# Kernel tuning notes

Hardware: AMD Instinct MI355X
Metric: run time of the kernel (lower is better)

Reference implementation:

```python
import jax, jax.numpy as jnp
import numpy as np

N_NODES = 100000
N_EDGES = 1600000
NUM_FEATURES = 256
HIDDEN_DIM = 128
NUM_CLASSES = 16


def setup_inputs() -> dict:
    key = jax.random.key(0)
    k1, k2, k3, k4 = jax.random.split(key, 4)
    x = jax.random.normal(k1, (N_NODES, NUM_FEATURES), dtype=jnp.float32)
    edge_index = jax.random.randint(k2, (2, N_EDGES), 0, N_NODES, dtype=jnp.int64)
    # Glorot-style init like PyG GCNConv's Linear
    W1 = jax.random.normal(k3, (NUM_FEATURES, HIDDEN_DIM), dtype=jnp.float32) / np.sqrt(NUM_FEATURES)
    b1 = jnp.zeros((HIDDEN_DIM,), dtype=jnp.float32)
    W2 = jax.random.normal(k4, (HIDDEN_DIM, NUM_CLASSES), dtype=jnp.float32) / np.sqrt(HIDDEN_DIM)
    b2 = jnp.zeros((NUM_CLASSES,), dtype=jnp.float32)
    return {"x": x, "edge_index": edge_index, "W1": W1, "b1": b1, "W2": W2, "b2": b2}


def _gcn_norm(edge_index, num_nodes):
    """PyG GCNConv default: add self-loops, symmetric deg^{-1/2} A deg^{-1/2} norm."""
    loops = jnp.arange(num_nodes, dtype=edge_index.dtype)
    row = jnp.concatenate([edge_index[0], loops])  # source
    col = jnp.concatenate([edge_index[1], loops])  # target
    deg = jax.ops.segment_sum(jnp.ones_like(col, dtype=jnp.float32), col,
                              num_segments=num_nodes)
    dinv = jnp.where(deg > 0, jax.lax.rsqrt(deg), 0.0)
    norm = dinv[row] * dinv[col]  # [E + N]
    return row, col, norm


def _gcn_conv(h, row, col, norm, num_nodes):
    # transform first (PyG: lin then propagate), then normalized sum-aggregate
    msg = h[row] * norm[:, None]            # [E+N, d] gather + scale
    return jax.ops.segment_sum(msg, col, num_segments=num_nodes)


def reference(x, edge_index, W1, b1, W2, b2):
    num_nodes = x.shape[0]
    row, col, norm = _gcn_norm(edge_index, num_nodes)
    h = x @ W1
    h = _gcn_conv(h, row, col, norm, num_nodes) + b1
    h = jax.nn.relu(h)
    h = h @ W2
    out = _gcn_conv(h, row, col, norm, num_nodes) + b2
    return out
```

## Files before the change

kernel.cpp:

```cpp
#include <hip/hip_runtime.h>

#define N_NODES 100000
#define N_EDGES 1600000
#define F_IN    256
#define F_HID   128
#define F_OUT   16

#define BSHIFT  9
#define BNODES  512
#define NB      196
#define ECAP    16384
#define CHUNK   4096
#define NCHUNK  ((N_EDGES + CHUNK - 1) / CHUNK)

typedef __attribute__((ext_vector_type(8))) short short8;
typedef __attribute__((ext_vector_type(4))) float float4v;

__device__ __forceinline__ unsigned int bf16_rn(float f) {
    unsigned int u = __float_as_uint(f);
    return (u + 0x7FFFu + ((u >> 16) & 1u)) >> 16;
}
__device__ __forceinline__ unsigned int cvtpk(float lo, float hi) {
    unsigned int r;
    asm("v_cvt_pk_bf16_f32 %0, %1, %2" : "=v"(r) : "v"(lo), "v"(hi));
    return r;
}
__device__ __forceinline__ float blo(unsigned int u) { return __uint_as_float(u << 16); }
__device__ __forceinline__ float bhi(unsigned int u) { return __uint_as_float(u & 0xFFFF0000u); }
__device__ __forceinline__ float bfu(unsigned short u) { return __uint_as_float(((unsigned int)u) << 16); }


__global__ __launch_bounds__(256) void k_binit(int* __restrict__ bcur) {
    int i = threadIdx.x;
    if (i < NB) bcur[i] = i * ECAP;
}

__global__ __launch_bounds__(256) void k_binscatter(const int* __restrict__ rowi,
                                                    const int* __restrict__ coli,
                                                    int* __restrict__ bcur,
                                                    unsigned int* __restrict__ ebuf) {
    __shared__ int cnt[NB], gbase[NB], run[NB];
    int tid = threadIdx.x;
    int e0 = blockIdx.x * CHUNK;
    for (int i = tid; i < NB; i += 256) { cnt[i] = 0; run[i] = 0; }
    __syncthreads();
    int d[16], s[16];
    #pragma unroll
    for (int i = 0; i < 16; i++) {
        int e = e0 + i * 256 + tid;
        if (e < N_EDGES) {
            d[i] = coli[e]; s[i] = rowi[e];
            atomicAdd(&cnt[d[i] >> BSHIFT], 1);
        } else d[i] = -1;
    }
    __syncthreads();
    for (int i = tid; i < NB; i += 256)
        gbase[i] = cnt[i] ? atomicAdd(&bcur[i], cnt[i]) : 0;
    __syncthreads();
    #pragma unroll
    for (int i = 0; i < 16; i++) {
        if (d[i] >= 0) {
            int b = d[i] >> BSHIFT;
            int off = atomicAdd(&run[b], 1);
            ebuf[gbase[b] + off] = ((unsigned int)(d[i] & 511) << 17) | (unsigned int)s[i];
        }
    }
}

__global__ __launch_bounds__(512) void k_finalize(const int* __restrict__ bcur,
                                                  const unsigned int* __restrict__ ebuf,
                                                  int* __restrict__ rp_start,
                                                  int* __restrict__ rp_end,
                                                  float* __restrict__ dinv,
                                                  int* __restrict__ esrc) {
    __shared__ int ndeg[BNODES];
    __shared__ int sc[BNODES];
    int tid = threadIdx.x;
    int b   = blockIdx.x;
    int nb0 = b << BSHIFT;
    int ebeg = b * ECAP, eend = bcur[b];
    ndeg[tid] = 0;
    __syncthreads();
    for (int e = ebeg + tid; e < eend; e += 512)
        atomicAdd(&ndeg[ebuf[e] >> 17], 1);
    __syncthreads();
    sc[tid] = ndeg[tid];
    __syncthreads();
    for (int off = 1; off < BNODES; off <<= 1) {
        int v = (tid >= off) ? sc[tid - off] : 0;
        __syncthreads();
        sc[tid] += v;
        __syncthreads();
    }
    {
        int n = nb0 + tid;
        int deg = ndeg[tid];
        int excl = sc[tid] - deg;
        if (n < N_NODES) {
            rp_start[n] = ebeg + excl;
            rp_end[n]   = ebeg + excl + deg;
            dinv[n]     = rsqrtf(1.0f + (float)deg);
        }
        ndeg[tid] = excl;
    }
    __syncthreads();
    for (int e = ebeg + tid; e < eend; e += 512) {
        unsigned int p = ebuf[e];
        int off = atomicAdd(&ndeg[p >> 17], 1);
        esrc[ebeg + off] = (int)(p & 0x1FFFFu);
    }
}


__global__ __launch_bounds__(256) void k_transW(const float* __restrict__ W1,
                                                ushort* __restrict__ Wt) {
    int t = blockIdx.x * 256 + threadIdx.x;
    int c = t & 127, k = t >> 7;
    Wt[c * 256 + k] = (ushort)cvtpk(W1[k * 128 + c], 0.f);
}


__global__ __launch_bounds__(256) void k_gemm1(const float* __restrict__ x,
                                               const ushort* __restrict__ Wt,
                                               const float* __restrict__ dinv,
                                               ushort* __restrict__ g1) {
    __shared__ ushort Bl[128 * 256];
    const int tid = threadIdx.x;
    const int w = tid >> 6;
    const int l = tid & 63;
    const int m = l & 15;
    const int q = l >> 4;
    const int R0 = blockIdx.x * 128;

    {
        const uint4* Wg = (const uint4*)Wt;
        uint4* Bl4 = (uint4*)Bl;
        #pragma unroll
        for (int it = 0; it < 16; it++) {
            int i = it * 256 + tid;
            int c = i >> 5, j = i & 31;
            Bl4[c * 32 + (j ^ (c & 7))] = Wg[i];
        }
    }
    __syncthreads();

    int r0 = R0 + w * 32 + m;      if (r0 > N_NODES - 1) r0 = N_NODES - 1;
    int r1 = R0 + w * 32 + 16 + m; if (r1 > N_NODES - 1) r1 = N_NODES - 1;
    const float* xr0 = &x[(size_t)r0 * F_IN + q * 8];
    const float* xr1 = &x[(size_t)r1 * F_IN + q * 8];
    const short8* Bl8 = (const short8*)Bl;

    float4v acc[2][8];
    #pragma unroll
    for (int i = 0; i < 2; i++)
        #pragma unroll
        for (int j = 0; j < 8; j++) acc[i][j] = (float4v){0.f, 0.f, 0.f, 0.f};

    #pragma unroll 2
    for (int kt = 0; kt < F_IN; kt += 32) {
        float4 a0 = *(const float4*)&xr0[kt];
        float4 a1 = *(const float4*)&xr0[kt + 4];
        float4 b0 = *(const float4*)&xr1[kt];
        float4 b1 = *(const float4*)&xr1[kt + 4];
        short8 af0, af1;
        ((uint*)&af0)[0] = cvtpk(a0.x, a0.y); ((uint*)&af0)[1] = cvtpk(a0.z, a0.w);
        ((uint*)&af0)[2] = cvtpk(a1.x, a1.y); ((uint*)&af0)[3] = cvtpk(a1.z, a1.w);
        ((uint*)&af1)[0] = cvtpk(b0.x, b0.y); ((uint*)&af1)[1] = cvtpk(b0.z, b0.w);
        ((uint*)&af1)[2] = cvtpk(b1.x, b1.y); ((uint*)&af1)[3] = cvtpk(b1.z, b1.w);
        int jq = (kt >> 3) + q;
        #pragma unroll
        for (int n = 0; n < 8; n++) {
            int col = n * 16 + m;
            short8 bfr = Bl8[col * 32 + (jq ^ (col & 7))];
            acc[0][n] = __builtin_amdgcn_mfma_f32_16x16x32_bf16(af0, bfr, acc[0][n], 0, 0, 0);
            acc[1][n] = __builtin_amdgcn_mfma_f32_16x16x32_bf16(af1, bfr, acc[1][n], 0, 0, 0);
        }
    }

    const int rbase = R0 + w * 32 + q * 4;
    float dv0[4], dv1[4];
    #pragma unroll
    for (int r = 0; r < 4; r++) {
        int v0 = rbase + r;      dv0[r] = (v0 < N_NODES) ? dinv[v0] : 0.f;
        int v1 = rbase + 16 + r; dv1[r] = (v1 < N_NODES) ? dinv[v1] : 0.f;
    }
    #pragma unroll
    for (int n = 0; n < 8; n++) {
        #pragma unroll
        for (int r = 0; r < 4; r++) {
            int v0 = rbase + r;
            if (v0 < N_NODES) {
                float f = dv0[r] * acc[0][n][r];
                g1[v0 * F_HID + n * 16 + m] = (ushort)cvtpk(f, f);
            }
            int v1 = rbase + 16 + r;
            if (v1 < N_NODES) {
                float f = dv1[r] * acc[1][n][r];
                g1[v1 * F_HID + n * 16 + m] = (ushort)cvtpk(f, f);
            }
        }
    }
}


__global__ __launch_bounds__(256) void k_agg1g2(const int* __restrict__ rp_start,
                                                const int* __restrict__ rp_end,
                                                const int* __restrict__ esrc,
                                                const float* __restrict__ dinv,
                                                const unsigned int* __restrict__ g1,
                                                const float* __restrict__ b1,
                                                const float* __restrict__ W2,
                                                ushort* __restrict__ g2b,
                                                int nbase) {
    __shared__ float hl[4][132];
    const int tid  = threadIdx.x;
    const int wave = tid >> 6;
    const int lane = tid & 63;
    const int col  = lane & 15, part = lane >> 4;

    float w2r[32];
    #pragma unroll
    for (int i = 0; i < 32; i++) w2r[i] = W2[i * 64 + lane];

    float2 bb = ((const float2*)b1)[lane];

    #pragma unroll 1
    for (int j = 0; j < 4; j++) {
        const int node = nbase + blockIdx.x * 16 + j * 4 + wave;
        int s = rp_start[node], t = rp_end[node];
        unsigned int u = g1[node * 64 + lane];
        float ax = blo(u), ay = bhi(u);
        int e = s;
        for (; e + 7 < t; e += 8) {
            int r0 = esrc[e],     r1 = esrc[e + 1], r2 = esrc[e + 2], r3 = esrc[e + 3];
            int r4 = esrc[e + 4], r5 = esrc[e + 5], r6 = esrc[e + 6], r7 = esrc[e + 7];
            unsigned int u0 = g1[r0 * 64 + lane], u1 = g1[r1 * 64 + lane];
            unsigned int u2 = g1[r2 * 64 + lane], u3 = g1[r3 * 64 + lane];
            unsigned int u4 = g1[r4 * 64 + lane], u5 = g1[r5 * 64 + lane];
            unsigned int u6 = g1[r6 * 64 + lane], u7 = g1[r7 * 64 + lane];
            ax += blo(u0) + blo(u1) + blo(u2) + blo(u3)
                + blo(u4) + blo(u5) + blo(u6) + blo(u7);
            ay += bhi(u0) + bhi(u1) + bhi(u2) + bhi(u3)
                + bhi(u4) + bhi(u5) + bhi(u6) + bhi(u7);
        }
        for (; e + 3 < t; e += 4) {
            int r0 = esrc[e], r1 = esrc[e + 1], r2 = esrc[e + 2], r3 = esrc[e + 3];
            unsigned int u0 = g1[r0 * 64 + lane], u1 = g1[r1 * 64 + lane];
            unsigned int u2 = g1[r2 * 64 + lane], u3 = g1[r3 * 64 + lane];
            ax += blo(u0) + blo(u1) + blo(u2) + blo(u3);
            ay += bhi(u0) + bhi(u1) + bhi(u2) + bhi(u3);
        }
        for (; e < t; e++) {
            unsigned int u0 = g1[esrc[e] * 64 + lane];
            ax += blo(u0); ay += bhi(u0);
        }
        float wv = dinv[node];
        hl[wave][lane * 2]     = fmaxf(fmaf(wv, ax, bb.x), 0.0f);
        hl[wave][lane * 2 + 1] = fmaxf(fmaf(wv, ay, bb.y), 0.0f);

        float acc = 0.f;
        #pragma unroll
        for (int i = 0; i < 32; i++)
            acc = fmaf(hl[wave][i * 4 + part], w2r[i], acc);
        acc += __shfl_xor(acc, 16);
        acc += __shfl_xor(acc, 32);
        if (lane < 16) g2b[node * 16 + col] = (ushort)bf16_rn(wv * acc);
    }
}


__global__ __launch_bounds__(256) void k_agg2(const int* __restrict__ rp_start,
                                              const int* __restrict__ rp_end,
                                              const int* __restrict__ esrc,
                                              const float* __restrict__ dinv,
                                              const ushort* __restrict__ g2b,
                                              const float* __restrict__ b2,
                                              float* __restrict__ out) {
    int gid = blockIdx.x * 256 + threadIdx.x;
    int node = gid >> 4;
    int f = gid & 15;
    if (node >= N_NODES) return;
    int s = rp_start[node], t = rp_end[node];
    float acc = bfu(g2b[node * 16 + f]);
    int e = s;
    for (; e + 7 < t; e += 8) {
        float a0 = bfu(g2b[esrc[e] * 16 + f]),     a1 = bfu(g2b[esrc[e + 1] * 16 + f]);
        float a2 = bfu(g2b[esrc[e + 2] * 16 + f]), a3 = bfu(g2b[esrc[e + 3] * 16 + f]);
        float a4 = bfu(g2b[esrc[e + 4] * 16 + f]), a5 = bfu(g2b[esrc[e + 5] * 16 + f]);
        float a6 = bfu(g2b[esrc[e + 6] * 16 + f]), a7 = bfu(g2b[esrc[e + 7] * 16 + f]);
        acc += a0 + a1 + a2 + a3 + a4 + a5 + a6 + a7;
    }
    for (; e + 3 < t; e += 4) {
        acc += bfu(g2b[esrc[e] * 16 + f]) + bfu(g2b[esrc[e + 1] * 16 + f])
             + bfu(g2b[esrc[e + 2] * 16 + f]) + bfu(g2b[esrc[e + 3] * 16 + f]);
    }
    for (; e < t; e++) acc += bfu(g2b[esrc[e] * 16 + f]);
    out[node * 16 + f] = fmaf(dinv[node], acc, b2[f]);
}


extern "C" void kernel_launch(void* const* d_in, const int* in_sizes, int n_in,
                              void* d_out, int out_size, void* d_ws, size_t ws_size,
                              hipStream_t stream) {
    const float* x   = (const float*)d_in[0];
    const int*   ei  = (const int*)d_in[1];
    const float* W1  = (const float*)d_in[2];
    const float* b1  = (const float*)d_in[3];
    const float* W2  = (const float*)d_in[4];
    const float* b2  = (const float*)d_in[5];
    float* out = (float*)d_out;

    const int* rowi = ei;
    const int* coli = ei + N_EDGES;

    char* ws = (char*)d_ws;
    int*          bcur     = (int*)(ws + 0);
    int*          rp_start = (int*)(ws + 8192);
    int*          rp_end   = (int*)(ws + 524288);
    float*        dinv     = (float*)(ws + 1048576);
    unsigned int* ebuf     = (unsigned int*)(ws + 2097152);
    int*          esrc     = (int*)(ws + 16777216);
    ushort*       Wt       = (ushort*)(ws + 31457280);
    ushort*       g1       = (ushort*)(ws + 33554432);
    ushort*       g2b      = (ushort*)(ws + 62914560);

    k_binit     <<<1, 256, 0, stream>>>(bcur);
    k_binscatter<<<NCHUNK, 256, 0, stream>>>(rowi, coli, bcur, ebuf);
    k_finalize  <<<NB, 512, 0, stream>>>(bcur, ebuf, rp_start, rp_end, dinv, esrc);
    k_transW    <<<128, 256, 0, stream>>>(W1, Wt);

    k_gemm1     <<<(N_NODES + 127) / 128, 256, 0, stream>>>(x, Wt, dinv, g1);
    k_agg1g2    <<<N_NODES / 32, 256, 0, stream>>>(rp_start, rp_end, esrc, dinv,
                                                   (const unsigned int*)g1, b1, W2, g2b, 0);
    k_agg1g2    <<<N_NODES / 32, 256, 0, stream>>>(rp_start, rp_end, esrc, dinv,
                                                   (const unsigned int*)g1, b1, W2, g2b,
                                                   N_NODES / 2);
    k_agg2      <<<(N_NODES * 16 + 255) / 256, 256, 0, stream>>>(rp_start, rp_end, esrc,
                                                                 dinv, g2b, b2, out);
}
```

Measured before the change: 327.9 us.

## Stage x tiles into LDS with async double-buffered loads, keep W1 in registers

The first GEMM now streams x tiles into a double-buffered, XOR-swizzled LDS buffer using global_load_lds, prefetching the next K slice while MFMAs run on the current one. Each wave holds its 32-column slice of W1 in registers instead of staging all of W1 in LDS, and the work is repartitioned so each wave covers all 128 rows for 32 output columns. The aim is to hide the x-load latency and shrink LDS use so more blocks fit per CU. The cost is a barrier per K step and higher register pressure from the 16 W fragments plus 16 accumulators.

```diff
diff --git a/kernel.cpp b/kernel.cpp
--- a/kernel.cpp
+++ b/kernel.cpp
@@ -15,6 +15,9 @@
 
 typedef __attribute__((ext_vector_type(8))) short short8;
 typedef __attribute__((ext_vector_type(4))) float float4v;
+
+typedef __attribute__((address_space(1))) const void g_void;
+typedef __attribute__((address_space(3))) void lds_void;
 
 __device__ __forceinline__ unsigned int bf16_rn(float f) {
     unsigned int u = __float_as_uint(f);
@@ -124,79 +127,80 @@
                                                const ushort* __restrict__ Wt,
                                                const float* __restrict__ dinv,
                                                ushort* __restrict__ g1) {
-    __shared__ ushort Bl[128 * 256];
+    __shared__ float lx[2][128][32];
     const int tid = threadIdx.x;
-    const int w = tid >> 6;
-    const int l = tid & 63;
-    const int m = l & 15;
-    const int q = l >> 4;
+    const int wv = tid >> 6;
+    const int l  = tid & 63;
+    const int m  = l & 15;
+    const int q  = l >> 4;
     const int R0 = blockIdx.x * 128;
 
-    {
-        const uint4* Wg = (const uint4*)Wt;
-        uint4* Bl4 = (uint4*)Bl;
+    #pragma unroll
+    for (int r = 0; r < 4; r++) {
+        int rt = r * 32 + wv * 8 + (l >> 3);
+        int c16 = l & 7;
+        int grow = R0 + rt; if (grow > N_NODES - 1) grow = N_NODES - 1;
+        const float* src = x + (size_t)grow * F_IN + ((c16 ^ (rt & 7)) << 2);
+        float* dst = &lx[0][r * 32 + wv * 8][0];
+        __builtin_amdgcn_global_load_lds((g_void*)src, (lds_void*)dst, 16, 0, 0);
+    }
+
+    short8 wf[2][8];
+    #pragma unroll
+    for (int ng = 0; ng < 2; ng++)
         #pragma unroll
-        for (int it = 0; it < 16; it++) {
-            int i = it * 256 + tid;
-            int c = i >> 5, j = i & 31;
-            Bl4[c * 32 + (j ^ (c & 7))] = Wg[i];
-        }
-    }
-    __syncthreads();
-
-    int r0 = R0 + w * 32 + m;      if (r0 > N_NODES - 1) r0 = N_NODES - 1;
-    int r1 = R0 + w * 32 + 16 + m; if (r1 > N_NODES - 1) r1 = N_NODES - 1;
-    const float* xr0 = &x[(size_t)r0 * F_IN + q * 8];
-    const float* xr1 = &x[(size_t)r1 * F_IN + q * 8];
-    const short8* Bl8 = (const short8*)Bl;
-
-    float4v acc[2][8];
-    #pragma unroll
-    for (int i = 0; i < 2; i++)
+        for (int kt = 0; kt < 8; kt++)
+            wf[ng][kt] = *(const short8*)&Wt[(wv * 32 + ng * 16 + m) * 256 + kt * 32 + q * 8];
+
+    float4v acc[8][2];
+    #pragma unroll
+    for (int rg = 0; rg < 8; rg++) {
+        acc[rg][0] = (float4v){0.f, 0.f, 0.f, 0.f};
+        acc[rg][1] = (float4v){0.f, 0.f, 0.f, 0.f};
+    }
+
+    __syncthreads();
+
+    #pragma unroll
+    for (int kt = 0; kt < 8; kt++) {
+        const int buf = kt & 1;
+        if (kt < 7) {
+            #pragma unroll
+            for (int r = 0; r < 4; r++) {
+                int rt = r * 32 + wv * 8 + (l >> 3);
+                int c16 = l & 7;
+                int grow = R0 + rt; if (grow > N_NODES - 1) grow = N_NODES - 1;
+                const float* src = x + (size_t)grow * F_IN + (kt + 1) * 32
+                                     + ((c16 ^ (rt & 7)) << 2);
+                float* dst = &lx[buf ^ 1][r * 32 + wv * 8][0];
+                __builtin_amdgcn_global_load_lds((g_void*)src, (lds_void*)dst, 16, 0, 0);
+            }
+        }
         #pragma unroll
-        for (int j = 0; j < 8; j++) acc[i][j] = (float4v){0.f, 0.f, 0.f, 0.f};
-
-    #pragma unroll 2
-    for (int kt = 0; kt < F_IN; kt += 32) {
-        float4 a0 = *(const float4*)&xr0[kt];
-        float4 a1 = *(const float4*)&xr0[kt + 4];
-        float4 b0 = *(const float4*)&xr1[kt];
-        float4 b1 = *(const float4*)&xr1[kt + 4];
-        short8 af0, af1;
-        ((uint*)&af0)[0] = cvtpk(a0.x, a0.y); ((uint*)&af0)[1] = cvtpk(a0.z, a0.w);
-        ((uint*)&af0)[2] = cvtpk(a1.x, a1.y); ((uint*)&af0)[3] = cvtpk(a1.z, a1.w);
-        ((uint*)&af1)[0] = cvtpk(b0.x, b0.y); ((uint*)&af1)[1] = cvtpk(b0.z, b0.w);
-        ((uint*)&af1)[2] = cvtpk(b1.x, b1.y); ((uint*)&af1)[3] = cvtpk(b1.z, b1.w);
-        int jq = (kt >> 3) + q;
-        #pragma unroll
-        for (int n = 0; n < 8; n++) {
-            int col = n * 16 + m;
-            short8 bfr = Bl8[col * 32 + (jq ^ (col & 7))];
-            acc[0][n] = __builtin_amdgcn_mfma_f32_16x16x32_bf16(af0, bfr, acc[0][n], 0, 0, 0);
-            acc[1][n] = __builtin_amdgcn_mfma_f32_16x16x32_bf16(af1, bfr, acc[1][n], 0, 0, 0);
-        }
-    }
-
-    const int rbase = R0 + w * 32 + q * 4;
-    float dv0[4], dv1[4];
-    #pragma unroll
-    for (int r = 0; r < 4; r++) {
-        int v0 = rbase + r;      dv0[r] = (v0 < N_NODES) ? dinv[v0] : 0.f;
-        int v1 = rbase + 16 + r; dv1[r] = (v1 < N_NODES) ? dinv[v1] : 0.f;
-    }
-    #pragma unroll
-    for (int n = 0; n < 8; n++) {
+        for (int rg = 0; rg < 8; rg++) {
+            int rt = rg * 16 + m, sw = rt & 7;
+            float4 e0 = *(const float4*)&lx[buf][rt][((2 * q)     ^ sw) * 4];
+            float4 e1 = *(const float4*)&lx[buf][rt][((2 * q + 1) ^ sw) * 4];
+            short8 af;
+            ((uint*)&af)[0] = cvtpk(e0.x, e0.y); ((uint*)&af)[1] = cvtpk(e0.z, e0.w);
+            ((uint*)&af)[2] = cvtpk(e1.x, e1.y); ((uint*)&af)[3] = cvtpk(e1.z, e1.w);
+            acc[rg][0] = __builtin_amdgcn_mfma_f32_16x16x32_bf16(af, wf[0][kt], acc[rg][0], 0, 0, 0);
+            acc[rg][1] = __builtin_amdgcn_mfma_f32_16x16x32_bf16(af, wf[1][kt], acc[rg][1], 0, 0, 0);
+        }
+        __syncthreads();
+    }
+
+    #pragma unroll
+    for (int rg = 0; rg < 8; rg++) {
         #pragma unroll
         for (int r = 0; r < 4; r++) {
-            int v0 = rbase + r;
-            if (v0 < N_NODES) {
-                float f = dv0[r] * acc[0][n][r];
-                g1[v0 * F_HID + n * 16 + m] = (ushort)cvtpk(f, f);
-            }
-            int v1 = rbase + 16 + r;
-            if (v1 < N_NODES) {
-                float f = dv1[r] * acc[1][n][r];
-                g1[v1 * F_HID + n * 16 + m] = (ushort)cvtpk(f, f);
+            int row = R0 + rg * 16 + q * 4 + r;
+            if (row < N_NODES) {
+                float dv = dinv[row];
+                float f0 = dv * acc[rg][0][r];
+                float f1 = dv * acc[rg][1][r];
+                g1[row * F_HID + wv * 32 + m]      = (ushort)cvtpk(f0, f0);
+                g1[row * F_HID + wv * 32 + 16 + m] = (ushort)cvtpk(f1, f1);
             }
         }
     }
```

New measurement: 328.6 us. About the same (+0.2%).
